# Kernel tuning notes

Hardware: AMD Instinct MI355X
Metric: run time of the kernel (lower is better)

## Reference

```python
import jax, jax.numpy as jnp
import numpy as np

B, T, IN_DIM = 128, 512, 32
H = 256            # h_dim; bidirectional -> embedding_dim D = 2*H = 512
N_EMB = 1024
BETA = 0.25


def setup_inputs() -> dict:
    key = jax.random.key(0)
    ks = jax.random.split(key, 12)
    traj = jax.random.normal(ks[0], (B, T, IN_DIM), dtype=jnp.float32)
    # variable-length padding mask: ones up to length, zeros after
    lengths = jax.random.randint(ks[1], (B,), 1, T + 1)
    mask = (jnp.arange(T)[None, :] < lengths[:, None]).astype(jnp.int32)
    s_x = 1.0 / np.sqrt(H)
    def u(k, shape):
        return jax.random.uniform(k, shape, jnp.float32, -s_x, s_x)
    # PyTorch GRU param layout: W_ih [3H, in], W_hh [3H, H], biases [3H]
    Wx_f, Wh_f = u(ks[2], (3 * H, IN_DIM)), u(ks[3], (3 * H, H))
    bx_f, bh_f = u(ks[4], (3 * H,)), u(ks[5], (3 * H,))
    Wx_b, Wh_b = u(ks[6], (3 * H, IN_DIM)), u(ks[7], (3 * H, H))
    bx_b, bh_b = u(ks[8], (3 * H,)), u(ks[9], (3 * H,))
    # codebook: nn.Embedding(n_embeddings, D) with uniform(-1/n, 1/n) init
    codebook = jax.random.uniform(ks[10], (N_EMB, 2 * H), jnp.float32,
                                  -1.0 / N_EMB, 1.0 / N_EMB)
    return {"traj": traj, "mask": mask,
            "Wx_f": Wx_f, "Wh_f": Wh_f, "bx_f": bx_f, "bh_f": bh_f,
            "Wx_b": Wx_b, "Wh_b": Wh_b, "bx_b": bx_b, "bh_b": bh_b,
            "codebook": codebook}


def _gru_dir(x, Wx, Wh, bx, bh):
    """Single-direction GRU over time (PyTorch gate math). x: [B,T,in] -> [B,T,H]."""
    b, t, _ = x.shape
    h_dim = Wh.shape[1]
    xg = jnp.einsum('bti,gi->btg', x, Wx) + bx  # precompute input gates [B,T,3H]
    def step(h, xg_t):
        hg = h @ Wh.T + bh
        xr, xz, xn = jnp.split(xg_t, 3, axis=-1)
        hr, hz, hn = jnp.split(hg, 3, axis=-1)
        r = jax.nn.sigmoid(xr + hr)
        z = jax.nn.sigmoid(xz + hz)
        n = jnp.tanh(xn + r * hn)
        h_new = (1.0 - z) * n + z * h
        return h_new, h_new
    h0 = jnp.zeros((b, h_dim), x.dtype)
    _, hs = jax.lax.scan(step, h0, jnp.swapaxes(xg, 0, 1))  # [T,B,H]
    return jnp.swapaxes(hs, 0, 1)


def _encode(traj, Wx_f, Wh_f, bx_f, bh_f, Wx_b, Wh_b, bx_b, bh_b):
    out_f = _gru_dir(traj, Wx_f, Wh_f, bx_f, bh_f)
    out_b = jnp.flip(_gru_dir(jnp.flip(traj, axis=1), Wx_b, Wh_b, bx_b, bh_b), axis=1)
    return jnp.concatenate([out_f, out_b], axis=-1)  # [B,T,2H]


def _vq(z_e, codebook, beta):
    # d(z, e) = |z|^2 + |e|^2 - 2 z.e  -> argmin over codebook
    d = (jnp.sum(z_e ** 2, axis=1, keepdims=True)
         + jnp.sum(codebook ** 2, axis=1)[None, :]
         - 2.0 * z_e @ codebook.T)                      # [B, N_EMB]
    idx = jnp.argmin(d, axis=1)                         # [B]
    z_q = codebook[idx]                                 # gather [B, D]
    loss = (jnp.mean((jax.lax.stop_gradient(z_q) - z_e) ** 2)
            + beta * jnp.mean((z_q - jax.lax.stop_gradient(z_e)) ** 2))
    z_q_st = z_e + jax.lax.stop_gradient(z_q - z_e)     # straight-through
    counts = jnp.zeros((codebook.shape[0],), z_e.dtype).at[idx].add(1.0)
    p = counts / z_e.shape[0]
    perplexity = jnp.exp(-jnp.sum(p * jnp.log(p + 1e-10)))
    return loss, z_q_st, perplexity, idx


def reference(traj, mask, Wx_f, Wh_f, bx_f, bh_f, Wx_b, Wh_b, bx_b, bh_b, codebook):
    z_e = _encode(traj, Wx_f, Wh_f, bx_f, bh_f, Wx_b, Wh_b, bx_b, bh_b)  # [B,T,2H]
    t = mask.shape[1]
    # last index where mask == 1:  T-1 - argmax(flip(mask))
    last_real_index = t - 1 - jnp.argmax(jnp.flip(mask, axis=1), axis=1)
    z_e_last = z_e[jnp.arange(z_e.shape[0]), last_real_index]            # [B,2H]
    loss, z_q, perplexity, _ = _vq(z_e_last, codebook, BETA)
    return z_q, loss, perplexity
```

## Files before the change

### kernel.cpp

```cpp
#include <hip/hip_runtime.h>
#include <math.h>

constexpr int B  = 128;
constexpr int T  = 512;
constexpr int IN = 32;
constexpr int H  = 256;
constexpr int D  = 2 * H;
constexpr int NC = 1024;

constexpr int NG   = 64;
constexpr int GW   = 4;
constexpr int SEQ  = 4;
constexpr int NTHR = 768;

constexpr int LDS_PAD_BYTES = 28672;


__global__ void k_zero(int* __restrict__ counts, double* __restrict__ lsum,
                       unsigned long long* __restrict__ slab) {
    const int i = blockIdx.x * 256 + threadIdx.x;
    if (i < NC) counts[i] = 0;
    if (i == 0) *lsum = 0.0;
    slab[i] = 0ull;
}

__global__ void k_lengths(const int* __restrict__ mask, int* __restrict__ last) {
    const int b = blockIdx.x;
    const int t = threadIdx.x;
    int s = 0;
    #pragma unroll
    for (int m = 0; m < T / 64; ++m) s += mask[b * T + m * 64 + t];
    #pragma unroll
    for (int off = 32; off > 0; off >>= 1) s += __shfl_down(s, off, 64);
    if (t == 0) last[b] = s - 1;
}

__global__ void k_plan(const int* __restrict__ last, int* __restrict__ plan,
                       int* __restrict__ slen, int* __restrict__ glen) {
    __shared__ int ll[B];
    const int t = threadIdx.x;
    ll[t] = last[t];
    __syncthreads();
    const int lf = ll[t] + 1;
    const int lb = T - ll[t];
    int rf = 0, rb = 0;
    for (int j = 0; j < B; ++j) {
        const int ljf = ll[j] + 1, ljb = T - ll[j];
        rf += (ljf > lf) || (ljf == lf && j < t);
        rb += (ljb > lb) || (ljb == lb && j < t);
    }
    plan[rf] = t;       slen[rf] = lf;
    plan[128 + rb] = t; slen[128 + rb] = lb;
    if ((rf & 3) == 0) glen[rf >> 2] = lf;
    if ((rb & 3) == 0) glen[32 + (rb >> 2)] = lb;
}

__global__ void k_transpose(float* __restrict__ dst, const float* __restrict__ src,
                            int rows, int cols) {
    const int idx = blockIdx.x * 256 + threadIdx.x;
    const int r = idx % rows;
    const int c = idx / rows;
    dst[idx] = src[r * cols + c];
}

__global__ void k_cbn2(const float* __restrict__ cb, double* __restrict__ cbn2) {
    const int c = blockIdx.x * 256 + threadIdx.x;
    double s = 0.0;
    for (int k = 0; k < D; ++k) {
        const double e = (double)cb[c * D + k];
        s += e * e;
    }
    cbn2[c] = s;
}


__device__ __forceinline__ float sigmoidf_(float x) {
    return 1.0f / (1.0f + expf(-x));
}

__global__ __launch_bounds__(NTHR, 3) void k_gru(
    const float* __restrict__ traj,
    const float* __restrict__ Whf, const float* __restrict__ Whb,
    const float* __restrict__ Wxf, const float* __restrict__ Wxb,
    const float* __restrict__ bxf, const float* __restrict__ bhf,
    const float* __restrict__ bxb, const float* __restrict__ bhb,
    const int* __restrict__ plan, const int* __restrict__ slen,
    const int* __restrict__ glen,
    unsigned long long* __restrict__ hgt,
    float* __restrict__ ze)
{
    extern __shared__ float dynpad[];
    (void)dynpad;

    const int g   = blockIdx.x & 63;
    const int w   = blockIdx.x >> 6;
    const int dir = (g >= 32) ? 1 : 0;

    const float* __restrict__ Wh = dir ? Whb : Whf;
    const float* __restrict__ Wx = dir ? Wxb : Wxf;
    const float* __restrict__ bx = dir ? bxb : bxf;
    const float* __restrict__ bh = dir ? bhb : bhf;

    const int tid = threadIdx.x;
    const int kq  = tid / 96;
    const int rp  = tid - kq * 96;
    const int lr0 = 2 * rp;
    const int gi  = lr0 >> 6;
    const int Rg0 = gi * H + w * 64 + (lr0 & 63);

    __shared__ float4 h4[SEQ][64];
    __shared__ float  P [8][SEQ][194];
    __shared__ float  Px[8][SEQ][194];
    __shared__ float4 xb4[2][SEQ][8];
    __shared__ int    bbS[SEQ], lsS[SEQ];

    if (tid < SEQ) { bbS[tid] = plan[g * 4 + tid]; lsS[tid] = slen[g * 4 + tid]; }
    {
        float2* hp = (float2*)h4;
        if (tid < 512) hp[tid] = make_float2(0.0f, 0.0f);
    }
    const int L = glen[g];

    float4 wh[16];
    {
        const float4* p0 = (const float4*)(Wh + (size_t)Rg0 * 256 + kq * 32);
        const float4* p1 = (const float4*)(Wh + (size_t)(Rg0 + 1) * 256 + kq * 32);
        #pragma unroll
        for (int i = 0; i < 8; ++i) { wh[i] = p0[i]; wh[8 + i] = p1[i]; }
    }
    const float4 wx0 = *(const float4*)(Wx + Rg0 * 32 + kq * 4);
    const float4 wx1 = *(const float4*)(Wx + (Rg0 + 1) * 32 + kq * 4);

    float bxr = 0, bxz = 0, bxn = 0, bhr = 0, bhz = 0, bhn = 0;
    if (tid < 256) {
        const int j2 = tid & 63;
        bxr = bx[w * 64 + j2]; bxz = bx[H + w * 64 + j2]; bxn = bx[2 * H + w * 64 + j2];
        bhr = bh[w * 64 + j2]; bhz = bh[H + w * 64 + j2]; bhn = bh[2 * H + w * 64 + j2];
    }
    __syncthreads();
    if (tid < 128) {
        const int s = tid >> 5, i = tid & 31;
        const int t0 = dir ? (T - 1) : 0;
        ((float*)xb4)[128 + s * 32 + i] = traj[(bbS[s] * T + t0) * IN + i];
    }
    __syncthreads();

    const int u = tid - 256;

    for (int step = 1; step <= L; ++step) {
        const int buf = step & 1;
        unsigned long long* __restrict__ slab =
            hgt + (buf * NG + g) * (GW * SEQ * 64);

        float4 a0 = {0,0,0,0}, a1 = {0,0,0,0}, a2 = {0,0,0,0}, a3 = {0,0,0,0};
        float4 c0 = {0,0,0,0}, c1 = {0,0,0,0}, c2 = {0,0,0,0}, c3 = {0,0,0,0};
        #pragma unroll
        for (int i = 0; i < 8; ++i) {
            const float4 w0 = wh[i];
            const float4 w1 = wh[8 + i];
            float4 hv;
            hv = h4[0][kq * 8 + i];
            a0.x = fmaf(w0.x, hv.x, a0.x); a0.y = fmaf(w0.y, hv.y, a0.y);
            a0.z = fmaf(w0.z, hv.z, a0.z); a0.w = fmaf(w0.w, hv.w, a0.w);
            c0.x = fmaf(w1.x, hv.x, c0.x); c0.y = fmaf(w1.y, hv.y, c0.y);
            c0.z = fmaf(w1.z, hv.z, c0.z); c0.w = fmaf(w1.w, hv.w, c0.w);
            hv = h4[1][kq * 8 + i];
            a1.x = fmaf(w0.x, hv.x, a1.x); a1.y = fmaf(w0.y, hv.y, a1.y);
            a1.z = fmaf(w0.z, hv.z, a1.z); a1.w = fmaf(w0.w, hv.w, a1.w);
            c1.x = fmaf(w1.x, hv.x, c1.x); c1.y = fmaf(w1.y, hv.y, c1.y);
            c1.z = fmaf(w1.z, hv.z, c1.z); c1.w = fmaf(w1.w, hv.w, c1.w);
            hv = h4[2][kq * 8 + i];
            a2.x = fmaf(w0.x, hv.x, a2.x); a2.y = fmaf(w0.y, hv.y, a2.y);
            a2.z = fmaf(w0.z, hv.z, a2.z); a2.w = fmaf(w0.w, hv.w, a2.w);
            c2.x = fmaf(w1.x, hv.x, c2.x); c2.y = fmaf(w1.y, hv.y, c2.y);
            c2.z = fmaf(w1.z, hv.z, c2.z); c2.w = fmaf(w1.w, hv.w, c2.w);
            hv = h4[3][kq * 8 + i];
            a3.x = fmaf(w0.x, hv.x, a3.x); a3.y = fmaf(w0.y, hv.y, a3.y);
            a3.z = fmaf(w0.z, hv.z, a3.z); a3.w = fmaf(w0.w, hv.w, a3.w);
            c3.x = fmaf(w1.x, hv.x, c3.x); c3.y = fmaf(w1.y, hv.y, c3.y);
            c3.z = fmaf(w1.z, hv.z, c3.z); c3.w = fmaf(w1.w, hv.w, c3.w);
        }
        {
            float4 xv;
            float2 pv;
            xv = xb4[buf][0][kq];
            pv.x = a0.x + a0.y + a0.z + a0.w;
            pv.y = c0.x + c0.y + c0.z + c0.w;
            *(float2*)&P[kq][0][lr0] = pv;
            pv.x = wx0.x * xv.x + wx0.y * xv.y + wx0.z * xv.z + wx0.w * xv.w;
            pv.y = wx1.x * xv.x + wx1.y * xv.y + wx1.z * xv.z + wx1.w * xv.w;
            *(float2*)&Px[kq][0][lr0] = pv;
            xv = xb4[buf][1][kq];
            pv.x = a1.x + a1.y + a1.z + a1.w;
            pv.y = c1.x + c1.y + c1.z + c1.w;
            *(float2*)&P[kq][1][lr0] = pv;
            pv.x = wx0.x * xv.x + wx0.y * xv.y + wx0.z * xv.z + wx0.w * xv.w;
            pv.y = wx1.x * xv.x + wx1.y * xv.y + wx1.z * xv.z + wx1.w * xv.w;
            *(float2*)&Px[kq][1][lr0] = pv;
            xv = xb4[buf][2][kq];
            pv.x = a2.x + a2.y + a2.z + a2.w;
            pv.y = c2.x + c2.y + c2.z + c2.w;
            *(float2*)&P[kq][2][lr0] = pv;
            pv.x = wx0.x * xv.x + wx0.y * xv.y + wx0.z * xv.z + wx0.w * xv.w;
            pv.y = wx1.x * xv.x + wx1.y * xv.y + wx1.z * xv.z + wx1.w * xv.w;
            *(float2*)&Px[kq][2][lr0] = pv;
            xv = xb4[buf][3][kq];
            pv.x = a3.x + a3.y + a3.z + a3.w;
            pv.y = c3.x + c3.y + c3.z + c3.w;
            *(float2*)&P[kq][3][lr0] = pv;
            pv.x = wx0.x * xv.x + wx0.y * xv.y + wx0.z * xv.z + wx0.w * xv.w;
            pv.y = wx1.x * xv.x + wx1.y * xv.y + wx1.z * xv.z + wx1.w * xv.w;
            *(float2*)&Px[kq][3][lr0] = pv;
        }
        __syncthreads();

        if (tid < 256) {
            float xval = 0.0f;
            int xs = 0, xi = 0;
            const bool do_x = (tid < 128) && (step < L);
            if (do_x) {
                xs = tid >> 5; xi = tid & 31;
                const int tn = dir ? (T - 1 - step) : step;
                xval = traj[(bbS[xs] * T + tn) * IN + xi];
            }
            const int j2 = tid & 63, s = tid >> 6;
            float hr = 0.f, hz = 0.f, hn_ = 0.f, xr = 0.f, xz = 0.f, xn = 0.f;
            #pragma unroll
            for (int kk = 0; kk < 8; ++kk) {
                hr  += P [kk][s][j2];
                hz  += P [kk][s][64 + j2];
                hn_ += P [kk][s][128 + j2];
                xr  += Px[kk][s][j2];
                xz  += Px[kk][s][64 + j2];
                xn  += Px[kk][s][128 + j2];
            }
            const float r = sigmoidf_(xr + bxr + hr + bhr);
            const float z = sigmoidf_(xz + bxz + hz + bhz);
            const float n = tanhf(xn + bxn + r * (hn_ + bhn));
            const int jg = w * 64 + j2;
            const float hp = ((const float*)h4)[s * 256 + jg];
            const float hnew = (1.0f - z) * n + z * hp;
            ((float*)h4)[s * 256 + jg] = hnew;
            union { float f; unsigned ui; } cv; cv.f = hnew;
            const unsigned long long pk =
                ((unsigned long long)(unsigned)step << 32) | cv.ui;
            __hip_atomic_store(&slab[w * 256 + s * 64 + j2], pk,
                               __ATOMIC_RELAXED, __HIP_MEMORY_SCOPE_AGENT);
            if (step == lsS[s]) ze[bbS[s] * D + dir * H + jg] = hnew;
            const int pw0 = (0 >= w) ? 1 : 0;
            unsigned long long* ad0 = &slab[pw0 * 256 + s * 64 + j2];
            unsigned long long v0;
            do {
                v0 = __hip_atomic_load(ad0, __ATOMIC_RELAXED,
                                       __HIP_MEMORY_SCOPE_AGENT);
            } while ((int)(v0 >> 32) < step);
            union { unsigned ui; float f; } e0; e0.ui = (unsigned)v0;
            ((float*)h4)[s * 256 + pw0 * 64 + j2] = e0.f;
            if (do_x)
                ((float*)xb4)[(buf ^ 1) * 128 + xs * 32 + xi] = xval;
        } else {
            const int pi = 1 + (u >> 8);
            const int r2 = u & 255;
            const int s0 = r2 >> 6, j0 = r2 & 63;
            const int pw0 = pi + (pi >= w ? 1 : 0);
            unsigned long long* ad0 = &slab[pw0 * 256 + s0 * 64 + j0];
            unsigned long long v0;
            do {
                v0 = __hip_atomic_load(ad0, __ATOMIC_RELAXED,
                                       __HIP_MEMORY_SCOPE_AGENT);
            } while ((int)(v0 >> 32) < step);
            union { unsigned ui; float f; } e0; e0.ui = (unsigned)v0;
            ((float*)h4)[s0 * 256 + pw0 * 64 + j0] = e0.f;
        }
        __syncthreads();
    }
}


__global__ __launch_bounds__(256) void k_vq(
    const float* __restrict__ ze, const float* __restrict__ cbT,
    const float* __restrict__ cb, const double* __restrict__ cbn2,
    int* __restrict__ counts, double* __restrict__ lsum,
    float* __restrict__ out)
{
    __shared__ float lz[D];
    __shared__ double ds[256];
    __shared__ int cs[256];

    const int b = blockIdx.x;
    const int t = threadIdx.x;

    lz[t]       = ze[b * D + t];
    lz[t + 256] = ze[b * D + 256 + t];
    __syncthreads();

    double best = 1e300;
    int bc = 0;
    for (int m = 0; m < NC / 256; ++m) {
        const int c = m * 256 + t;
        double s2 = 0.0;
        #pragma unroll 4
        for (int k = 0; k < D; ++k)
            s2 += (double)lz[k] * (double)cbT[k * NC + c];
        const double dist = cbn2[c] - 2.0 * s2;
        if (dist < best) { best = dist; bc = c; }
    }
    ds[t] = best; cs[t] = bc;
    __syncthreads();
    for (int s = 128; s > 0; s >>= 1) {
        if (t < s) {
            if (ds[t + s] < ds[t] || (ds[t + s] == ds[t] && cs[t + s] < cs[t])) {
                ds[t] = ds[t + s]; cs[t] = cs[t + s];
            }
        }
        __syncthreads();
    }
    const int idx = cs[0];
    __syncthreads();

    if (t == 0) atomicAdd(&counts[idx], 1);

    double loc = 0.0;
    for (int jj = t; jj < D; jj += 256) {
        const float zev = lz[jj];
        const float zqv = cb[idx * D + jj];
        out[b * D + jj] = zev + (zqv - zev);
        const double df = (double)zqv - (double)zev;
        loc += df * df;
    }
    ds[t] = loc;
    __syncthreads();
    for (int s = 128; s > 0; s >>= 1) {
        if (t < s) ds[t] += ds[t + s];
        __syncthreads();
    }
    if (t == 0) atomicAdd(lsum, ds[0]);
}

__global__ void k_final(const int* __restrict__ counts,
                        const double* __restrict__ lsum,
                        float* __restrict__ out)
{
    __shared__ double ds[256];
    const int t = threadIdx.x;
    double s = 0.0;
    for (int c = t; c < NC; c += 256) {
        const double p = (double)counts[c] / (double)B;
        s += p * log(p + 1e-10);
    }
    ds[t] = s;
    __syncthreads();
    for (int r = 128; r > 0; r >>= 1) {
        if (t < r) ds[t] += ds[t + r];
        __syncthreads();
    }
    if (t == 0) {
        out[B * D]     = (float)(lsum[0] * 1.25 / (double)(B * D));
        out[B * D + 1] = (float)exp(-ds[0]);
    }
}


extern "C" void kernel_launch(void* const* d_in, const int* in_sizes, int n_in,
                              void* d_out, int out_size, void* d_ws, size_t ws_size,
                              hipStream_t stream) {
    const float* traj = (const float*)d_in[0];
    const int*   mask = (const int*)d_in[1];
    const float* Wxf  = (const float*)d_in[2];
    const float* Whf  = (const float*)d_in[3];
    const float* bxf  = (const float*)d_in[4];
    const float* bhf  = (const float*)d_in[5];
    const float* Wxb  = (const float*)d_in[6];
    const float* Whb  = (const float*)d_in[7];
    const float* bxb  = (const float*)d_in[8];
    const float* bhb  = (const float*)d_in[9];
    const float* cb   = (const float*)d_in[10];
    float* out = (float*)d_out;

    float* ws    = (float*)d_ws;
    float* cbT   = ws;
    float* zebuf = cbT + 524288;
    unsigned long long* hgt =
        (unsigned long long*)(zebuf + 65536);
    int*   last  = (int*)(hgt + 131072);
    int*   plan  = last + 128;
    int*   slen  = plan + 256;
    int*   glen  = slen + 256;
    int*   cnts  = glen + 64;
    double* cbn2 = (double*)(cnts + 1024 + 4);
    double* lsum = cbn2 + 1024;

    k_zero<<<dim3(512), dim3(256), 0, stream>>>(cnts, lsum, hgt);
    k_lengths<<<dim3(B), dim3(64), 0, stream>>>(mask, last);
    k_plan<<<dim3(1), dim3(B), 0, stream>>>(last, plan, slen, glen);

    k_transpose<<<dim3(2048), dim3(256), 0, stream>>>(cbT, cb, NC, D);
    k_cbn2<<<dim3(4), dim3(256), 0, stream>>>(cb, cbn2);

    k_gru<<<dim3(NG * GW), dim3(NTHR), LDS_PAD_BYTES, stream>>>(
        traj, Whf, Whb, Wxf, Wxb, bxf, bhf, bxb, bhb,
        plan, slen, glen, hgt, zebuf);

    k_vq<<<dim3(B), dim3(256), 0, stream>>>(zebuf, cbT, cb, cbn2, cnts, lsum, out);
    k_final<<<dim3(1), dim3(256), 0, stream>>>(cnts, lsum, out);
}
```

Before: 1.694 ms.

## Merge small prep kernels and fold final reduction into VQ via last-block flag

Combines the mask-length and plan kernels into one single-block kernel, merges the codebook transpose (now LDS-tiled) with the norm computation in one launch, and removes the final perplexity kernel by having the last-finishing VQ block, detected with an atomic counter, compute the loss and perplexity. The aim is to cut kernel launch count and launch gaps around the long GRU kernel. The trade-off is extra atomics and a serial tail inside the VQ kernel, plus a single-block prep kernel that reads the whole mask serially per thread.

```diff
diff --git a/kernel.cpp b/kernel.cpp
--- a/kernel.cpp
+++ b/kernel.cpp
@@ -17,60 +17,74 @@
 
 
 __global__ void k_zero(int* __restrict__ counts, double* __restrict__ lsum,
+                       int* __restrict__ done,
                        unsigned long long* __restrict__ slab) {
     const int i = blockIdx.x * 256 + threadIdx.x;
     if (i < NC) counts[i] = 0;
-    if (i == 0) *lsum = 0.0;
+    if (i == 0) { *lsum = 0.0; *done = 0; }
     slab[i] = 0ull;
 }
 
-__global__ void k_lengths(const int* __restrict__ mask, int* __restrict__ last) {
-    const int b = blockIdx.x;
-    const int t = threadIdx.x;
-    int s = 0;
-    #pragma unroll
-    for (int m = 0; m < T / 64; ++m) s += mask[b * T + m * 64 + t];
-    #pragma unroll
-    for (int off = 32; off > 0; off >>= 1) s += __shfl_down(s, off, 64);
-    if (t == 0) last[b] = s - 1;
-}
-
-__global__ void k_plan(const int* __restrict__ last, int* __restrict__ plan,
-                       int* __restrict__ slen, int* __restrict__ glen) {
+__global__ void k_prep(const int* __restrict__ mask,
+                       int* __restrict__ plan, int* __restrict__ slen,
+                       int* __restrict__ glen) {
     __shared__ int ll[B];
     const int t = threadIdx.x;
-    ll[t] = last[t];
-    __syncthreads();
-    const int lf = ll[t] + 1;
-    const int lb = T - ll[t];
-    int rf = 0, rb = 0;
-    for (int j = 0; j < B; ++j) {
-        const int ljf = ll[j] + 1, ljb = T - ll[j];
-        rf += (ljf > lf) || (ljf == lf && j < t);
-        rb += (ljb > lb) || (ljb == lb && j < t);
-    }
-    plan[rf] = t;       slen[rf] = lf;
-    plan[128 + rb] = t; slen[128 + rb] = lb;
-    if ((rf & 3) == 0) glen[rf >> 2] = lf;
-    if ((rb & 3) == 0) glen[32 + (rb >> 2)] = lb;
-}
-
-__global__ void k_transpose(float* __restrict__ dst, const float* __restrict__ src,
-                            int rows, int cols) {
-    const int idx = blockIdx.x * 256 + threadIdx.x;
-    const int r = idx % rows;
-    const int c = idx / rows;
-    dst[idx] = src[r * cols + c];
-}
-
-__global__ void k_cbn2(const float* __restrict__ cb, double* __restrict__ cbn2) {
-    const int c = blockIdx.x * 256 + threadIdx.x;
-    double s = 0.0;
-    for (int k = 0; k < D; ++k) {
-        const double e = (double)cb[c * D + k];
-        s += e * e;
-    }
-    cbn2[c] = s;
+    {
+        const int b = t >> 2, q = t & 3;
+        const int* mp = mask + b * T + q * 128;
+        int s = 0;
+        #pragma unroll
+        for (int i = 0; i < 128; ++i) s += mp[i];
+        s += __shfl_xor(s, 1, 64);
+        s += __shfl_xor(s, 2, 64);
+        if (q == 0) ll[b] = s - 1;
+    }
+    __syncthreads();
+    if (t < B) {
+        const int lf = ll[t] + 1;
+        const int lb = T - ll[t];
+        int rf = 0, rb = 0;
+        for (int j = 0; j < B; ++j) {
+            const int ljf = ll[j] + 1, ljb = T - ll[j];
+            rf += (ljf > lf) || (ljf == lf && j < t);
+            rb += (ljb > lb) || (ljb == lb && j < t);
+        }
+        plan[rf] = t;       slen[rf] = lf;
+        plan[128 + rb] = t; slen[128 + rb] = lb;
+        if ((rf & 3) == 0) glen[rf >> 2] = lf;
+        if ((rb & 3) == 0) glen[32 + (rb >> 2)] = lb;
+    }
+}
+
+__global__ void k_tc(float* __restrict__ cbT, const float* __restrict__ cb,
+                     double* __restrict__ cbn2) {
+    const int bid = blockIdx.x;
+    if (bid < 512) {
+        __shared__ float tile[32][33];
+        const int tc = bid & 31;
+        const int tk = bid >> 5;
+        const int tx = threadIdx.x & 31, ty4 = threadIdx.x >> 5;
+        #pragma unroll
+        for (int j = 0; j < 4; ++j) {
+            const int ty = ty4 * 4 + j;
+            tile[ty][tx] = cb[(tc * 32 + ty) * D + tk * 32 + tx];
+        }
+        __syncthreads();
+        #pragma unroll
+        for (int j = 0; j < 4; ++j) {
+            const int ty = ty4 * 4 + j;
+            cbT[(tk * 32 + ty) * NC + tc * 32 + tx] = tile[tx][ty];
+        }
+    } else {
+        const int c = (bid - 512) * 256 + threadIdx.x;
+        double s = 0.0;
+        for (int k = 0; k < D; ++k) {
+            const double e = (double)cb[c * D + k];
+            s += e * e;
+        }
+        cbn2[c] = s;
+    }
 }
 
 
@@ -281,11 +295,13 @@
     const float* __restrict__ ze, const float* __restrict__ cbT,
     const float* __restrict__ cb, const double* __restrict__ cbn2,
     int* __restrict__ counts, double* __restrict__ lsum,
+    int* __restrict__ done,
     float* __restrict__ out)
 {
     __shared__ float lz[D];
     __shared__ double ds[256];
     __shared__ int cs[256];
+    __shared__ int lastFlag;
 
     const int b = blockIdx.x;
     const int t = threadIdx.x;
@@ -335,28 +351,34 @@
         __syncthreads();
     }
     if (t == 0) atomicAdd(lsum, ds[0]);
-}
-
-__global__ void k_final(const int* __restrict__ counts,
-                        const double* __restrict__ lsum,
-                        float* __restrict__ out)
-{
-    __shared__ double ds[256];
-    const int t = threadIdx.x;
-    double s = 0.0;
-    for (int c = t; c < NC; c += 256) {
-        const double p = (double)counts[c] / (double)B;
-        s += p * log(p + 1e-10);
-    }
-    ds[t] = s;
-    __syncthreads();
-    for (int r = 128; r > 0; r >>= 1) {
-        if (t < r) ds[t] += ds[t + r];
-        __syncthreads();
-    }
+
     if (t == 0) {
-        out[B * D]     = (float)(lsum[0] * 1.25 / (double)(B * D));
-        out[B * D + 1] = (float)exp(-ds[0]);
+        const int prev = __hip_atomic_fetch_add(done, 1, __ATOMIC_ACQ_REL,
+                                                __HIP_MEMORY_SCOPE_AGENT);
+        lastFlag = (prev == B - 1);
+    }
+    __syncthreads();
+    if (lastFlag) {
+        double s = 0.0;
+        for (int c = t; c < NC; c += 256) {
+            const int cnt = __hip_atomic_load(&counts[c], __ATOMIC_RELAXED,
+                                              __HIP_MEMORY_SCOPE_AGENT);
+            const double p = (double)cnt / (double)B;
+            s += p * log(p + 1e-10);
+        }
+        ds[t] = s;
+        __syncthreads();
+        for (int r = 128; r > 0; r >>= 1) {
+            if (t < r) ds[t] += ds[t + r];
+            __syncthreads();
+        }
+        if (t == 0) {
+            union { unsigned long long u; double d; } lv;
+            lv.u = __hip_atomic_load((unsigned long long*)lsum,
+                                     __ATOMIC_RELAXED, __HIP_MEMORY_SCOPE_AGENT);
+            out[B * D]     = (float)(lv.d * 1.25 / (double)(B * D));
+            out[B * D + 1] = (float)exp(-ds[0]);
+        }
     }
 }
 
@@ -389,18 +411,16 @@
     int*   cnts  = glen + 64;
     double* cbn2 = (double*)(cnts + 1024 + 4);
     double* lsum = cbn2 + 1024;
-
-    k_zero<<<dim3(512), dim3(256), 0, stream>>>(cnts, lsum, hgt);
-    k_lengths<<<dim3(B), dim3(64), 0, stream>>>(mask, last);
-    k_plan<<<dim3(1), dim3(B), 0, stream>>>(last, plan, slen, glen);
-
-    k_transpose<<<dim3(2048), dim3(256), 0, stream>>>(cbT, cb, NC, D);
-    k_cbn2<<<dim3(4), dim3(256), 0, stream>>>(cb, cbn2);
+    int*   done  = (int*)(lsum + 1);
+
+    k_zero<<<dim3(512), dim3(256), 0, stream>>>(cnts, lsum, done, hgt);
+    k_prep<<<dim3(1), dim3(512), 0, stream>>>(mask, plan, slen, glen);
+    k_tc  <<<dim3(516), dim3(256), 0, stream>>>(cbT, cb, cbn2);
 
     k_gru<<<dim3(NG * GW), dim3(NTHR), LDS_PAD_BYTES, stream>>>(
         traj, Whf, Whb, Wxf, Wxb, bxf, bhf, bxb, bhb,
         plan, slen, glen, hgt, zebuf);
 
-    k_vq<<<dim3(B), dim3(256), 0, stream>>>(zebuf, cbT, cb, cbn2, cnts, lsum, out);
-    k_final<<<dim3(1), dim3(256), 0, stream>>>(cnts, lsum, out);
-}
+    k_vq<<<dim3(B), dim3(256), 0, stream>>>(zebuf, cbT, cb, cbn2, cnts, lsum,
+                                            done, out);
+}
```

Result: no change. 1.702 ms, median of 2 (+0.5%).
